# Kernel tuning notes

Measured on AMD Instinct MI355X. Metric: run time of the kernel, lower is better.

Reference implementation:

```python
import jax, jax.numpy as jnp
import numpy as np

N_WIRES = 24
DIM = 2
N_LAYERS = 4  # brickwork layers -> 12+11+12+11 = 46 two-qubit gates


def _brick_pairs():
    pairs = []
    for layer in range(N_LAYERS):
        start = layer % 2
        for w in range(start, N_WIRES - 1, 2):
            pairs.append((w, w + 1))
    return np.asarray(pairs, dtype=np.int64)  # (46, 2)


def setup_inputs() -> dict:
    key = jax.random.key(0)
    k1, k2 = jax.random.split(key)
    gate_wires = _brick_pairs()
    n_gates = gate_wires.shape[0]
    # per-wire initial state vectors (AbstractState -> one free index per wire)
    states = jax.random.normal(k1, (N_WIRES, DIM), dtype=jnp.float32)
    # two-qubit gates, axis order (in0, out0, in1, out1) per subscripts_unitary
    gates = jax.random.normal(k2, (n_gates, DIM, DIM, DIM, DIM), dtype=jnp.float32)
    return {"states": states, "gates": gates, "gate_wires": gate_wires}


def reference(states, gates, gate_wires):
    # Equivalent to jnp.einsum(subscripts_unitary(circuit), *tensors):
    # outer-product of initial per-wire states, then sequential contraction
    # of each gate's input axes (0, 2) with the state's wire axes.
    n_wires = states.shape[0]
    wires = np.asarray(gate_wires)
    psi = states[0]
    for w in range(1, n_wires):  # fixed structural loop over wires
        psi = jnp.tensordot(psi, states[w], axes=0)  # -> (d,)*n_wires
    for g in range(gates.shape[0]):  # fixed structural loop over gates
        w0, w1 = int(wires[g, 0]), int(wires[g, 1])
        # gate axes: 0=in0, 1=out0, 2=in1, 3=out1
        psi = jnp.tensordot(gates[g], psi, axes=[[0, 2], [w0, w1]])
        # result axes: (out0, out1, remaining wires); restore wire ordering
        psi = jnp.moveaxis(psi, (0, 1), (w0, w1))
    return psi  # final statevector, shape (d,)*n_wires
```

## Files before the change

### kernel.cpp

```cpp
#include <hip/hip_runtime.h>
#include <hip/hip_bf16.h>


#define SWZ(j) ((j) ^ (((j) >> 6) & 15) ^ ((((j) >> 10) & 1) << 4))

template<int A>
__device__ __forceinline__ void gate_regs(float v[64], const float* __restrict__ g) {
  float m[16];
#pragma unroll
  for (int vv = 0; vv < 4; ++vv)
#pragma unroll
    for (int uu = 0; uu < 4; ++uu)
      m[vv * 4 + uu] = g[(uu >> 1) * 8 + (vv >> 1) * 4 + (uu & 1) * 2 + (vv & 1)];
  constexpr int S = 1 << A;
#pragma unroll
  for (int hi = 0; hi < (1 << (4 - A)); ++hi)
#pragma unroll
    for (int lo = 0; lo < S; ++lo) {
      const int base = (hi << (A + 2)) | lo;
      const float a0 = v[base], a1 = v[base + S], a2 = v[base + 2 * S], a3 = v[base + 3 * S];
      v[base]         = m[0]  * a0 + m[1]  * a1 + m[2]  * a2 + m[3]  * a3;
      v[base + S]     = m[4]  * a0 + m[5]  * a1 + m[6]  * a2 + m[7]  * a3;
      v[base + 2 * S] = m[8]  * a0 + m[9]  * a1 + m[10] * a2 + m[11] * a3;
      v[base + 3 * S] = m[12] * a0 + m[13] * a1 + m[14] * a2 + m[15] * a3;
    }
}

#define J_B(t, r)  (((r) << 8) | (t))
#define J_M(t, r)  ((((t) >> 4) << 10) | ((r) << 4) | ((t) & 15))
#define J_A(t, r)  (((t) << 6) | (r))
#define J_W(t, r)  ((((t) >> 5) << 11) | ((r) << 5) | ((t) & 31))

#define TRANSITION(JW, JR)                                   \
  do {                                                       \
    _Pragma("unroll")                                        \
    for (int r = 0; r < 64; ++r) tile[SWZ(JW(t, r))] = v[r]; \
    __syncthreads();                                         \
    _Pragma("unroll")                                        \
    for (int r = 0; r < 64; ++r) v[r] = tile[SWZ(JR(t, r))]; \
    __syncthreads();                                         \
  } while (0)

__global__ __launch_bounds__(256) void k_pass1(
    const float* __restrict__ states, const float* __restrict__ gates,
    float* __restrict__ out) {
  __shared__ float tile[16384];
  __shared__ float sLo[256];
  __shared__ float sHi[64];
  const int t = threadIdx.x;
  const int b = blockIdx.x;

  {
    float p = 1.f;
    for (int k = 0; k < 8; ++k) p *= states[(23 - k) * 2 + ((t >> k) & 1)];
    sLo[t] = p;
    if (t < 64) {
      float q = 1.f;
      for (int k = 0; k < 6; ++k) q *= states[(15 - k) * 2 + ((t >> k) & 1)];
      sHi[t] = q;
    }
  }
  float pref = 1.f;
  for (int k = 0; k < 10; ++k) pref *= states[(9 - k) * 2 + ((b >> k) & 1)];
  __syncthreads();

  float v[64];
  const float plT = pref * sLo[t];
#pragma unroll
  for (int r = 0; r < 64; ++r) v[r] = plT * sHi[r];

  gate_regs<4>(v, gates + 16 * 5);
  gate_regs<2>(v, gates + 16 * 6);
  gate_regs<0>(v, gates + 16 * 7);
  gate_regs<3>(v, gates + 16 * 17);
  gate_regs<1>(v, gates + 16 * 18);
  gate_regs<2>(v, gates + 16 * 29);

  TRANSITION(J_B, J_M);

  gate_regs<2>(v, gates + 16 * 8);
  gate_regs<0>(v, gates + 16 * 9);
  gate_regs<3>(v, gates + 16 * 19);
  gate_regs<1>(v, gates + 16 * 20);
  gate_regs<4>(v, gates + 16 * 30);
  gate_regs<2>(v, gates + 16 * 31);

  TRANSITION(J_M, J_A);

  gate_regs<2>(v, gates + 16 * 10);
  gate_regs<0>(v, gates + 16 * 11);
  gate_regs<3>(v, gates + 16 * 21);
  gate_regs<1>(v, gates + 16 * 22);
  gate_regs<4>(v, gates + 16 * 32);
  gate_regs<2>(v, gates + 16 * 33);
  gate_regs<0>(v, gates + 16 * 34);
  gate_regs<3>(v, gates + 16 * 44);
  gate_regs<1>(v, gates + 16 * 45);

  TRANSITION(J_A, J_W);

  gate_regs<4>(v, gates + 16 * 41);
  gate_regs<2>(v, gates + 16 * 42);
  gate_regs<0>(v, gates + 16 * 43);

  const long long ob = ((long long)b) << 14;
#pragma unroll
  for (int r = 0; r < 64; ++r) out[ob | J_W(t, r)] = v[r];
}

__global__ __launch_bounds__(256) void k_pass2a(
    const float* __restrict__ gates, float* __restrict__ out) {
  __shared__ float tile[16384];
  const int t = threadIdx.x;
  const int b = blockIdx.x;
  const long long base0 = (((long long)(b >> 4)) << 18) | ((long long)(b & 15) << 6);

  float v[64];
#pragma unroll
  for (int r = 0; r < 64; ++r) {
    const int j = J_B(t, r);
    v[r] = out[base0 | (((long long)(j >> 6)) << 10) | (j & 63)];
  }
  gate_regs<4>(v, gates + 16 * 3);
  gate_regs<2>(v, gates + 16 * 4);
  gate_regs<3>(v, gates + 16 * 15);
  gate_regs<1>(v, gates + 16 * 16);
  gate_regs<2>(v, gates + 16 * 27);
  gate_regs<0>(v, gates + 16 * 28);
  gate_regs<1>(v, gates + 16 * 39);

  TRANSITION(J_B, J_W);

  gate_regs<2>(v, gates + 16 * 40);

#pragma unroll
  for (int r = 0; r < 64; ++r) {
    const int j = J_W(t, r);
    out[base0 | (((long long)(j >> 6)) << 10) | (j & 63)] = v[r];
  }
}

__global__ __launch_bounds__(256) void k_pass2b(
    const float* __restrict__ gates, float* __restrict__ out) {
  __shared__ float tile[16384];
  const int t = threadIdx.x;
  const int b = blockIdx.x;

  float v[64];
#pragma unroll
  for (int r = 0; r < 64; ++r) {
    const int j = J_B(t, r);
    v[r] = out[(((long long)(j >> 5)) << 15) | ((long long)b << 5) | (j & 31)];
  }
  gate_regs<4>(v, gates + 16 * 0);
  gate_regs<2>(v, gates + 16 * 1);
  gate_regs<0>(v, gates + 16 * 2);
  gate_regs<3>(v, gates + 16 * 12);
  gate_regs<1>(v, gates + 16 * 13);
  gate_regs<4>(v, gates + 16 * 23);
  gate_regs<2>(v, gates + 16 * 24);
  gate_regs<3>(v, gates + 16 * 35);

  TRANSITION(J_B, J_W);

  gate_regs<2>(v, gates + 16 * 14);
  gate_regs<3>(v, gates + 16 * 25);
  gate_regs<1>(v, gates + 16 * 26);
  gate_regs<4>(v, gates + 16 * 36);
  gate_regs<2>(v, gates + 16 * 37);
  gate_regs<0>(v, gates + 16 * 38);

#pragma unroll
  for (int r = 0; r < 64; ++r) {
    const int j = J_W(t, r);
    out[(((long long)(j >> 5)) << 15) | ((long long)b << 5) | (j & 31)] = v[r];
  }
}

extern "C" void kernel_launch(void* const* d_in, const int* in_sizes, int n_in,
                              void* d_out, int out_size, void* d_ws, size_t ws_size,
                              hipStream_t stream) {
  const float* states = (const float*)d_in[0];
  const float* gates = (const float*)d_in[1];
  float* out = (float*)d_out;

  k_pass1<<<1024, 256, 0, stream>>>(states, gates, out);
  k_pass2a<<<1024, 256, 0, stream>>>(gates, out);
  k_pass2b<<<1024, 256, 0, stream>>>(gates, out);
}
```

Baseline: 201.2 us.

## Vectorize global loads/stores as float4 and use packed float2 gate math

Global reads and writes in all three passes now move 16 float4 values per thread instead of 64 scalar accesses. Extra shared-memory transitions (J_F, J_V layouts) are added so that each thread holds four contiguous low-index amplitudes, and gate applications are reordered across the transitions to match the new register layouts. The gate kernel is also rewritten to use two-wide float vectors, aiming at packed FMA instructions. This trades more LDS shuffles and barriers for wider, better-coalesced global traffic.

Measured after the change: 202.3 us. No clear change (+0.6%).

```diff
diff --git a/kernel.cpp b/kernel.cpp
--- a/kernel.cpp
+++ b/kernel.cpp
@@ -1,6 +1,8 @@
 #include <hip/hip_runtime.h>
 #include <hip/hip_bf16.h>
 
+
+typedef float v2f __attribute__((ext_vector_type(2)));
 
 #define SWZ(j) ((j) ^ (((j) >> 6) & 15) ^ ((((j) >> 10) & 1) << 4))
 
@@ -12,24 +14,45 @@
 #pragma unroll
     for (int uu = 0; uu < 4; ++uu)
       m[vv * 4 + uu] = g[(uu >> 1) * 8 + (vv >> 1) * 4 + (uu & 1) * 2 + (vv & 1)];
-  constexpr int S = 1 << A;
-#pragma unroll
-  for (int hi = 0; hi < (1 << (4 - A)); ++hi)
-#pragma unroll
-    for (int lo = 0; lo < S; ++lo) {
-      const int base = (hi << (A + 2)) | lo;
-      const float a0 = v[base], a1 = v[base + S], a2 = v[base + 2 * S], a3 = v[base + 3 * S];
-      v[base]         = m[0]  * a0 + m[1]  * a1 + m[2]  * a2 + m[3]  * a3;
-      v[base + S]     = m[4]  * a0 + m[5]  * a1 + m[6]  * a2 + m[7]  * a3;
-      v[base + 2 * S] = m[8]  * a0 + m[9]  * a1 + m[10] * a2 + m[11] * a3;
-      v[base + 3 * S] = m[12] * a0 + m[13] * a1 + m[14] * a2 + m[15] * a3;
+  if constexpr (A == 0) {
+    v2f m04 = {m[0], m[4]}, m15 = {m[1], m[5]}, m26 = {m[2], m[6]}, m37 = {m[3], m[7]};
+    v2f m8c = {m[8], m[12]}, m9d = {m[9], m[13]}, mae = {m[10], m[14]}, mbf = {m[11], m[15]};
+#pragma unroll
+    for (int q = 0; q < 16; ++q) {
+      const float a0 = v[4 * q], a1 = v[4 * q + 1], a2 = v[4 * q + 2], a3 = v[4 * q + 3];
+      v2f r01 = m04 * a0 + m15 * a1 + m26 * a2 + m37 * a3;
+      v2f r23 = m8c * a0 + m9d * a1 + mae * a2 + mbf * a3;
+      v[4 * q] = r01.x; v[4 * q + 1] = r01.y; v[4 * q + 2] = r23.x; v[4 * q + 3] = r23.y;
     }
+  } else {
+    constexpr int S = 1 << A;
+#pragma unroll
+    for (int hi = 0; hi < (1 << (4 - A)); ++hi)
+#pragma unroll
+      for (int lo2 = 0; lo2 < S / 2; ++lo2) {
+        const int base = (hi << (A + 2)) | (lo2 << 1);
+        v2f a0 = {v[base], v[base + 1]};
+        v2f a1 = {v[base + S], v[base + S + 1]};
+        v2f a2 = {v[base + 2 * S], v[base + 2 * S + 1]};
+        v2f a3 = {v[base + 3 * S], v[base + 3 * S + 1]};
+        v2f r0 = m[0] * a0 + m[1] * a1 + m[2] * a2 + m[3] * a3;
+        v2f r1 = m[4] * a0 + m[5] * a1 + m[6] * a2 + m[7] * a3;
+        v2f r2 = m[8] * a0 + m[9] * a1 + m[10] * a2 + m[11] * a3;
+        v2f r3 = m[12] * a0 + m[13] * a1 + m[14] * a2 + m[15] * a3;
+        v[base] = r0.x; v[base + 1] = r0.y;
+        v[base + S] = r1.x; v[base + S + 1] = r1.y;
+        v[base + 2 * S] = r2.x; v[base + 2 * S + 1] = r2.y;
+        v[base + 3 * S] = r3.x; v[base + 3 * S + 1] = r3.y;
+      }
+  }
 }
 
 #define J_B(t, r)  (((r) << 8) | (t))
 #define J_M(t, r)  ((((t) >> 4) << 10) | ((r) << 4) | ((t) & 15))
 #define J_A(t, r)  (((t) << 6) | (r))
 #define J_W(t, r)  ((((t) >> 5) << 11) | ((r) << 5) | ((t) & 31))
+#define J_F(t, r)  (((r) & 3) | ((t) << 2) | (((r) >> 2) << 10))
+#define J_V(t, r)  (((t) & 127) | ((r) << 7) | (((t) >> 7) << 13))
 
 #define TRANSITION(JW, JR)                                   \
   do {                                                       \
@@ -75,18 +98,14 @@
   gate_regs<3>(v, gates + 16 * 17);
   gate_regs<1>(v, gates + 16 * 18);
   gate_regs<2>(v, gates + 16 * 29);
-
   TRANSITION(J_B, J_M);
-
   gate_regs<2>(v, gates + 16 * 8);
   gate_regs<0>(v, gates + 16 * 9);
   gate_regs<3>(v, gates + 16 * 19);
   gate_regs<1>(v, gates + 16 * 20);
   gate_regs<4>(v, gates + 16 * 30);
   gate_regs<2>(v, gates + 16 * 31);
-
   TRANSITION(J_M, J_A);
-
   gate_regs<2>(v, gates + 16 * 10);
   gate_regs<0>(v, gates + 16 * 11);
   gate_regs<3>(v, gates + 16 * 21);
@@ -96,16 +115,18 @@
   gate_regs<0>(v, gates + 16 * 34);
   gate_regs<3>(v, gates + 16 * 44);
   gate_regs<1>(v, gates + 16 * 45);
-
   TRANSITION(J_A, J_W);
-
   gate_regs<4>(v, gates + 16 * 41);
   gate_regs<2>(v, gates + 16 * 42);
   gate_regs<0>(v, gates + 16 * 43);
+  TRANSITION(J_W, J_F);
 
   const long long ob = ((long long)b) << 14;
 #pragma unroll
-  for (int r = 0; r < 64; ++r) out[ob | J_W(t, r)] = v[r];
+  for (int c = 0; c < 16; ++c) {
+    float4 w = make_float4(v[4 * c], v[4 * c + 1], v[4 * c + 2], v[4 * c + 3]);
+    *(float4*)(&out[ob + (t << 2) + ((long long)c << 10)]) = w;
+  }
 }
 
 __global__ __launch_bounds__(256) void k_pass2a(
@@ -117,26 +138,25 @@
 
   float v[64];
 #pragma unroll
-  for (int r = 0; r < 64; ++r) {
-    const int j = J_B(t, r);
-    v[r] = out[base0 | (((long long)(j >> 6)) << 10) | (j & 63)];
+  for (int c = 0; c < 16; ++c) {
+    float4 x = *(const float4*)(&out[base0 + ((t & 15) << 2) + ((t >> 4) << 10) + ((long long)c << 14)]);
+    v[4 * c] = x.x; v[4 * c + 1] = x.y; v[4 * c + 2] = x.z; v[4 * c + 3] = x.w;
   }
   gate_regs<4>(v, gates + 16 * 3);
-  gate_regs<2>(v, gates + 16 * 4);
-  gate_regs<3>(v, gates + 16 * 15);
-  gate_regs<1>(v, gates + 16 * 16);
-  gate_regs<2>(v, gates + 16 * 27);
-  gate_regs<0>(v, gates + 16 * 28);
-  gate_regs<1>(v, gates + 16 * 39);
-
-  TRANSITION(J_B, J_W);
-
-  gate_regs<2>(v, gates + 16 * 40);
-
-#pragma unroll
-  for (int r = 0; r < 64; ++r) {
-    const int j = J_W(t, r);
-    out[base0 | (((long long)(j >> 6)) << 10) | (j & 63)] = v[r];
+  TRANSITION(J_F, J_V);
+  gate_regs<3>(v, gates + 16 * 4);
+  gate_regs<4>(v, gates + 16 * 15);
+  gate_regs<2>(v, gates + 16 * 16);
+  gate_regs<3>(v, gates + 16 * 27);
+  gate_regs<1>(v, gates + 16 * 28);
+  gate_regs<2>(v, gates + 16 * 39);
+  gate_regs<0>(v, gates + 16 * 40);
+  TRANSITION(J_V, J_F);
+
+#pragma unroll
+  for (int c = 0; c < 16; ++c) {
+    float4 w = make_float4(v[4 * c], v[4 * c + 1], v[4 * c + 2], v[4 * c + 3]);
+    *(float4*)(&out[base0 + ((t & 15) << 2) + ((t >> 4) << 10) + ((long long)c << 14)]) = w;
   }
 }
 
@@ -148,32 +168,32 @@
 
   float v[64];
 #pragma unroll
-  for (int r = 0; r < 64; ++r) {
-    const int j = J_B(t, r);
-    v[r] = out[(((long long)(j >> 5)) << 15) | ((long long)b << 5) | (j & 31)];
+  for (int c = 0; c < 16; ++c) {
+    float4 x = *(const float4*)(&out[((t & 7) << 2) + ((long long)b << 5) + ((t >> 3) << 15) + ((long long)c << 20)]);
+    v[4 * c] = x.x; v[4 * c + 1] = x.y; v[4 * c + 2] = x.z; v[4 * c + 3] = x.w;
   }
   gate_regs<4>(v, gates + 16 * 0);
   gate_regs<2>(v, gates + 16 * 1);
+  gate_regs<3>(v, gates + 16 * 12);
+  gate_regs<4>(v, gates + 16 * 23);
+  TRANSITION(J_F, J_B);
   gate_regs<0>(v, gates + 16 * 2);
-  gate_regs<3>(v, gates + 16 * 12);
   gate_regs<1>(v, gates + 16 * 13);
-  gate_regs<4>(v, gates + 16 * 23);
   gate_regs<2>(v, gates + 16 * 24);
   gate_regs<3>(v, gates + 16 * 35);
-
   TRANSITION(J_B, J_W);
-
   gate_regs<2>(v, gates + 16 * 14);
   gate_regs<3>(v, gates + 16 * 25);
   gate_regs<1>(v, gates + 16 * 26);
   gate_regs<4>(v, gates + 16 * 36);
   gate_regs<2>(v, gates + 16 * 37);
   gate_regs<0>(v, gates + 16 * 38);
-
-#pragma unroll
-  for (int r = 0; r < 64; ++r) {
-    const int j = J_W(t, r);
-    out[(((long long)(j >> 5)) << 15) | ((long long)b << 5) | (j & 31)] = v[r];
+  TRANSITION(J_W, J_F);
+
+#pragma unroll
+  for (int c = 0; c < 16; ++c) {
+    float4 w = make_float4(v[4 * c], v[4 * c + 1], v[4 * c + 2], v[4 * c + 3]);
+    *(float4*)(&out[((t & 7) << 2) + ((long long)b << 5) + ((t >> 3) << 15) + ((long long)c << 20)]) = w;
   }
 }
 
```

## Pack amplitudes into float2 vectors, halve LDS tile and vectorize global loads

Applied to the files above, without the earlier changes.

Stores each thread's 64 amplitudes as 32 float2 vectors so gate updates can use packed FMA instructions, with the qubit-to-register mappings remapped per stage. The LDS transpose is split into two half-sized rounds, which halves shared memory per block so that launch_bounds(256,4) can target four blocks per CU. The pass-2 kernels now load with float4 global reads and reorder gates across the transposes. The added barriers and extra LDS rounds add synchronisation cost, and the complex index remapping risks correctness errors.

New measurement: 261.7 us. 30.1% more time.

```diff
diff --git a/kernel.cpp b/kernel.cpp
--- a/kernel.cpp
+++ b/kernel.cpp
@@ -1,179 +1,213 @@
 #include <hip/hip_runtime.h>
-#include <hip/hip_bf16.h>
-
+
+
+typedef float v2f __attribute__((ext_vector_type(2)));
 
 #define SWZ(j) ((j) ^ (((j) >> 6) & 15) ^ ((((j) >> 10) & 1) << 4))
-
-template<int A>
-__device__ __forceinline__ void gate_regs(float v[64], const float* __restrict__ g) {
+#define DEL(x, S) (((x) & ((1 << (S)) - 1)) | (((x) >> ((S) + 1)) << (S)))
+#define AMP_LD(r) (((r) & 1) ? w[(r) >> 1].y : w[(r) >> 1].x)
+#define AMP_ST(r, val) do { if ((r) & 1) w[(r) >> 1].y = (val); else w[(r) >> 1].x = (val); } while (0)
+
+template<int B0, int B1>
+__device__ __forceinline__ void gate_v2(v2f w[32], const float* __restrict__ g) {
   float m[16];
 #pragma unroll
   for (int vv = 0; vv < 4; ++vv)
 #pragma unroll
     for (int uu = 0; uu < 4; ++uu)
       m[vv * 4 + uu] = g[(uu >> 1) * 8 + (vv >> 1) * 4 + (uu & 1) * 2 + (vv & 1)];
-  constexpr int S = 1 << A;
-#pragma unroll
-  for (int hi = 0; hi < (1 << (4 - A)); ++hi)
-#pragma unroll
-    for (int lo = 0; lo < S; ++lo) {
-      const int base = (hi << (A + 2)) | lo;
-      const float a0 = v[base], a1 = v[base + S], a2 = v[base + 2 * S], a3 = v[base + 3 * S];
-      v[base]         = m[0]  * a0 + m[1]  * a1 + m[2]  * a2 + m[3]  * a3;
-      v[base + S]     = m[4]  * a0 + m[5]  * a1 + m[6]  * a2 + m[7]  * a3;
-      v[base + 2 * S] = m[8]  * a0 + m[9]  * a1 + m[10] * a2 + m[11] * a3;
-      v[base + 3 * S] = m[12] * a0 + m[13] * a1 + m[14] * a2 + m[15] * a3;
-    }
-}
-
-#define J_B(t, r)  (((r) << 8) | (t))
-#define J_M(t, r)  ((((t) >> 4) << 10) | ((r) << 4) | ((t) & 15))
-#define J_A(t, r)  (((t) << 6) | (r))
-#define J_W(t, r)  ((((t) >> 5) << 11) | ((r) << 5) | ((t) & 31))
-
-#define TRANSITION(JW, JR)                                   \
-  do {                                                       \
-    _Pragma("unroll")                                        \
-    for (int r = 0; r < 64; ++r) tile[SWZ(JW(t, r))] = v[r]; \
-    __syncthreads();                                         \
-    _Pragma("unroll")                                        \
-    for (int r = 0; r < 64; ++r) v[r] = tile[SWZ(JR(t, r))]; \
-    __syncthreads();                                         \
+  if constexpr (B0 != 0 && B1 != 0) {
+    constexpr int S1 = 1 << B0, S0 = 1 << B1;
+#pragma unroll
+    for (int b = 0; b < 64; ++b) {
+      if (b & (S0 | S1 | 1)) continue;
+      v2f A0 = w[b >> 1], A1 = w[(b + S1) >> 1], A2 = w[(b + S0) >> 1], A3 = w[(b + S0 + S1) >> 1];
+      w[b >> 1]             = m[0] * A0 + m[1] * A1 + m[2] * A2 + m[3] * A3;
+      w[(b + S1) >> 1]      = m[4] * A0 + m[5] * A1 + m[6] * A2 + m[7] * A3;
+      w[(b + S0) >> 1]      = m[8] * A0 + m[9] * A1 + m[10] * A2 + m[11] * A3;
+      w[(b + S0 + S1) >> 1] = m[12] * A0 + m[13] * A1 + m[14] * A2 + m[15] * A3;
+    }
+  } else if constexpr (B0 == 0) {
+    constexpr int S0 = 1 << B1;
+    v2f m04 = {m[0], m[4]}, m15 = {m[1], m[5]}, m26 = {m[2], m[6]}, m37 = {m[3], m[7]};
+    v2f m8c = {m[8], m[12]}, m9d = {m[9], m[13]}, mae = {m[10], m[14]}, mbf = {m[11], m[15]};
+#pragma unroll
+    for (int b = 0; b < 64; ++b) {
+      if (b & (S0 | 1)) continue;
+      v2f p = w[b >> 1], q = w[(b + S0) >> 1];
+      w[b >> 1]        = m04 * p.x + m15 * p.y + m26 * q.x + m37 * q.y;
+      w[(b + S0) >> 1] = m8c * p.x + m9d * p.y + mae * q.x + mbf * q.y;
+    }
+  } else {
+    constexpr int S1 = 1 << B0;
+    v2f m08 = {m[0], m[8]}, m19 = {m[1], m[9]}, m2a = {m[2], m[10]}, m3b = {m[3], m[11]};
+    v2f m4c = {m[4], m[12]}, m5d = {m[5], m[13]}, m6e = {m[6], m[14]}, m7f = {m[7], m[15]};
+#pragma unroll
+    for (int b = 0; b < 64; ++b) {
+      if (b & (S1 | 1)) continue;
+      v2f p = w[b >> 1], q = w[(b + S1) >> 1];
+      w[b >> 1]        = m08 * p.x + m19 * q.x + m2a * p.y + m3b * q.y;
+      w[(b + S1) >> 1] = m4c * p.x + m5d * q.x + m6e * p.y + m7f * q.y;
+    }
+  }
+}
+
+#define JB1(t, r) ((t) | ((r) << 8))
+#define JM1(t, r) (((t) & 15) | ((((r) >> 1) & 15) << 4) | (((r) & 1) << 8) | (((r) >> 5) << 9) | (((t) >> 4) << 10))
+#define JA1(t, r) (((r) & 3) | ((((r) >> 3) & 7) << 2) | ((((r) >> 2) & 1) << 5) | ((t) << 6))
+#define JW1(t, r) (((t) & 31) | ((((r) >> 2) & 1) << 5) | (((r) & 1) << 6) | ((((r) >> 1) & 1) << 7) | ((((r) >> 3) & 7) << 8) | (((t) >> 5) << 11))
+#define JF(t, r)  (((r) & 3) | ((t) << 2) | (((r) >> 2) << 10))
+#define JV(t, r)  (((t) & 127) | (((r) & 1) << 7) | ((((r) >> 1) & 1) << 8) | ((((r) >> 3) & 1) << 9) | ((((r) >> 2) & 1) << 10) | ((((r) >> 4) & 3) << 11) | (((t) >> 7) << 13))
+#define JW2(t, r) (((t) & 31) | ((((r) >> 1) & 7) << 5) | (((r) & 1) << 8) | ((((r) >> 4) & 3) << 9) | (((t) >> 5) << 11))
+
+#define TRANS(JW, JR, S, RBIT)                                        \
+  do {                                                                \
+    _Pragma("unroll")                                                 \
+    for (int r = 0; r < 64; ++r) if ((((r) >> (RBIT)) & 1) == 0)      \
+      buf[DEL(SWZ(JW(t, r)), S)] = AMP_LD(r);                         \
+    __syncthreads();                                                  \
+    _Pragma("unroll")                                                 \
+    for (int r = 0; r < 64; ++r) if ((((r) >> (RBIT)) & 1) == 0)      \
+      AMP_ST(r, buf[DEL(SWZ(JR(t, r)), S)]);                          \
+    __syncthreads();                                                  \
+    _Pragma("unroll")                                                 \
+    for (int r = 0; r < 64; ++r) if ((((r) >> (RBIT)) & 1) == 1)      \
+      buf[DEL(SWZ(JW(t, r)), S)] = AMP_LD(r);                         \
+    __syncthreads();                                                  \
+    _Pragma("unroll")                                                 \
+    for (int r = 0; r < 64; ++r) if ((((r) >> (RBIT)) & 1) == 1)      \
+      AMP_ST(r, buf[DEL(SWZ(JR(t, r)), S)]);                          \
+    __syncthreads();                                                  \
   } while (0)
 
-__global__ __launch_bounds__(256) void k_pass1(
+__global__ __launch_bounds__(256, 4) void k_pass1(
     const float* __restrict__ states, const float* __restrict__ gates,
     float* __restrict__ out) {
-  __shared__ float tile[16384];
-  __shared__ float sLo[256];
-  __shared__ float sHi[64];
+  __shared__ float buf[8192];
   const int t = threadIdx.x;
   const int b = blockIdx.x;
 
   {
     float p = 1.f;
     for (int k = 0; k < 8; ++k) p *= states[(23 - k) * 2 + ((t >> k) & 1)];
-    sLo[t] = p;
+    buf[t] = p;
     if (t < 64) {
       float q = 1.f;
       for (int k = 0; k < 6; ++k) q *= states[(15 - k) * 2 + ((t >> k) & 1)];
-      sHi[t] = q;
+      buf[256 + t] = q;
     }
   }
   float pref = 1.f;
   for (int k = 0; k < 10; ++k) pref *= states[(9 - k) * 2 + ((b >> k) & 1)];
   __syncthreads();
 
-  float v[64];
-  const float plT = pref * sLo[t];
-#pragma unroll
-  for (int r = 0; r < 64; ++r) v[r] = plT * sHi[r];
-
-  gate_regs<4>(v, gates + 16 * 5);
-  gate_regs<2>(v, gates + 16 * 6);
-  gate_regs<0>(v, gates + 16 * 7);
-  gate_regs<3>(v, gates + 16 * 17);
-  gate_regs<1>(v, gates + 16 * 18);
-  gate_regs<2>(v, gates + 16 * 29);
-
-  TRANSITION(J_B, J_M);
-
-  gate_regs<2>(v, gates + 16 * 8);
-  gate_regs<0>(v, gates + 16 * 9);
-  gate_regs<3>(v, gates + 16 * 19);
-  gate_regs<1>(v, gates + 16 * 20);
-  gate_regs<4>(v, gates + 16 * 30);
-  gate_regs<2>(v, gates + 16 * 31);
-
-  TRANSITION(J_M, J_A);
-
-  gate_regs<2>(v, gates + 16 * 10);
-  gate_regs<0>(v, gates + 16 * 11);
-  gate_regs<3>(v, gates + 16 * 21);
-  gate_regs<1>(v, gates + 16 * 22);
-  gate_regs<4>(v, gates + 16 * 32);
-  gate_regs<2>(v, gates + 16 * 33);
-  gate_regs<0>(v, gates + 16 * 34);
-  gate_regs<3>(v, gates + 16 * 44);
-  gate_regs<1>(v, gates + 16 * 45);
-
-  TRANSITION(J_A, J_W);
-
-  gate_regs<4>(v, gates + 16 * 41);
-  gate_regs<2>(v, gates + 16 * 42);
-  gate_regs<0>(v, gates + 16 * 43);
+  v2f w[32];
+  const float plT = pref * buf[t];
+#pragma unroll
+  for (int i = 0; i < 32; ++i) {
+    w[i].x = plT * buf[256 + 2 * i];
+    w[i].y = plT * buf[256 + 2 * i + 1];
+  }
+  __syncthreads();
+
+  gate_v2<4, 5>(w, gates + 16 * 5);
+  gate_v2<2, 3>(w, gates + 16 * 6);
+  gate_v2<0, 1>(w, gates + 16 * 7);
+  gate_v2<3, 4>(w, gates + 16 * 17);
+  gate_v2<1, 2>(w, gates + 16 * 18);
+  gate_v2<2, 3>(w, gates + 16 * 29);
+  TRANS(JB1, JM1, 8, 0);
+  gate_v2<3, 4>(w, gates + 16 * 8);
+  gate_v2<1, 2>(w, gates + 16 * 9);
+  gate_v2<4, 0>(w, gates + 16 * 19);
+  gate_v2<2, 3>(w, gates + 16 * 20);
+  gate_v2<0, 5>(w, gates + 16 * 30);
+  gate_v2<3, 4>(w, gates + 16 * 31);
+  TRANS(JM1, JA1, 5, 2);
+  gate_v2<3, 4>(w, gates + 16 * 10);
+  gate_v2<0, 1>(w, gates + 16 * 11);
+  gate_v2<4, 5>(w, gates + 16 * 21);
+  gate_v2<1, 3>(w, gates + 16 * 22);
+  gate_v2<5, 2>(w, gates + 16 * 32);
+  gate_v2<3, 4>(w, gates + 16 * 33);
+  gate_v2<0, 1>(w, gates + 16 * 34);
+  gate_v2<4, 5>(w, gates + 16 * 44);
+  gate_v2<1, 3>(w, gates + 16 * 45);
+  TRANS(JA1, JW1, 5, 2);
+  gate_v2<4, 5>(w, gates + 16 * 41);
+  gate_v2<1, 3>(w, gates + 16 * 42);
+  gate_v2<2, 0>(w, gates + 16 * 43);
 
   const long long ob = ((long long)b) << 14;
 #pragma unroll
-  for (int r = 0; r < 64; ++r) out[ob | J_W(t, r)] = v[r];
-}
-
-__global__ __launch_bounds__(256) void k_pass2a(
+  for (int r = 0; r < 64; ++r) out[ob | JW1(t, r)] = AMP_LD(r);
+}
+
+__global__ __launch_bounds__(256, 4) void k_pass2a(
     const float* __restrict__ gates, float* __restrict__ out) {
-  __shared__ float tile[16384];
+  __shared__ float buf[8192];
   const int t = threadIdx.x;
   const int b = blockIdx.x;
   const long long base0 = (((long long)(b >> 4)) << 18) | ((long long)(b & 15) << 6);
 
-  float v[64];
+  v2f w[32];
+#pragma unroll
+  for (int c = 0; c < 16; ++c) {
+    float4 x = *(const float4*)(&out[base0 + ((t & 15) << 2) + ((t >> 4) << 10) + ((long long)c << 14)]);
+    w[2 * c] = (v2f){x.x, x.y};
+    w[2 * c + 1] = (v2f){x.z, x.w};
+  }
+  gate_v2<4, 5>(w, gates + 16 * 3);
+  TRANS(JF, JV, 10, 2);
+  gate_v2<2, 4>(w, gates + 16 * 4);
+  gate_v2<4, 5>(w, gates + 16 * 15);
+  gate_v2<3, 2>(w, gates + 16 * 16);
+  gate_v2<2, 4>(w, gates + 16 * 27);
+  gate_v2<1, 3>(w, gates + 16 * 28);
+  gate_v2<3, 2>(w, gates + 16 * 39);
+  gate_v2<0, 1>(w, gates + 16 * 40);
+
 #pragma unroll
   for (int r = 0; r < 64; ++r) {
-    const int j = J_B(t, r);
-    v[r] = out[base0 | (((long long)(j >> 6)) << 10) | (j & 63)];
-  }
-  gate_regs<4>(v, gates + 16 * 3);
-  gate_regs<2>(v, gates + 16 * 4);
-  gate_regs<3>(v, gates + 16 * 15);
-  gate_regs<1>(v, gates + 16 * 16);
-  gate_regs<2>(v, gates + 16 * 27);
-  gate_regs<0>(v, gates + 16 * 28);
-  gate_regs<1>(v, gates + 16 * 39);
-
-  TRANSITION(J_B, J_W);
-
-  gate_regs<2>(v, gates + 16 * 40);
-
-#pragma unroll
-  for (int r = 0; r < 64; ++r) {
-    const int j = J_W(t, r);
-    out[base0 | (((long long)(j >> 6)) << 10) | (j & 63)] = v[r];
-  }
-}
-
-__global__ __launch_bounds__(256) void k_pass2b(
+    const int j = JV(t, r);
+    out[base0 | (((long long)(j >> 6)) << 10) | (j & 63)] = AMP_LD(r);
+  }
+}
+
+__global__ __launch_bounds__(256, 4) void k_pass2b(
     const float* __restrict__ gates, float* __restrict__ out) {
-  __shared__ float tile[16384];
+  __shared__ float buf[8192];
   const int t = threadIdx.x;
   const int b = blockIdx.x;
 
-  float v[64];
+  v2f w[32];
+#pragma unroll
+  for (int c = 0; c < 16; ++c) {
+    float4 x = *(const float4*)(&out[((t & 7) << 2) + ((long long)b << 5) + ((t >> 3) << 15) + ((long long)c << 20)]);
+    w[2 * c] = (v2f){x.x, x.y};
+    w[2 * c + 1] = (v2f){x.z, x.w};
+  }
+  gate_v2<4, 5>(w, gates + 16 * 0);
+  gate_v2<2, 3>(w, gates + 16 * 1);
+  gate_v2<3, 4>(w, gates + 16 * 12);
+  gate_v2<4, 5>(w, gates + 16 * 23);
+  TRANS(JF, JB1, 10, 2);
+  gate_v2<0, 1>(w, gates + 16 * 2);
+  gate_v2<1, 2>(w, gates + 16 * 13);
+  gate_v2<2, 3>(w, gates + 16 * 24);
+  gate_v2<3, 4>(w, gates + 16 * 35);
+  TRANS(JB1, JW2, 8, 0);
+  gate_v2<3, 0>(w, gates + 16 * 14);
+  gate_v2<0, 4>(w, gates + 16 * 25);
+  gate_v2<2, 3>(w, gates + 16 * 26);
+  gate_v2<4, 5>(w, gates + 16 * 36);
+  gate_v2<3, 0>(w, gates + 16 * 37);
+  gate_v2<1, 2>(w, gates + 16 * 38);
+
 #pragma unroll
   for (int r = 0; r < 64; ++r) {
-    const int j = J_B(t, r);
-    v[r] = out[(((long long)(j >> 5)) << 15) | ((long long)b << 5) | (j & 31)];
-  }
-  gate_regs<4>(v, gates + 16 * 0);
-  gate_regs<2>(v, gates + 16 * 1);
-  gate_regs<0>(v, gates + 16 * 2);
-  gate_regs<3>(v, gates + 16 * 12);
-  gate_regs<1>(v, gates + 16 * 13);
-  gate_regs<4>(v, gates + 16 * 23);
-  gate_regs<2>(v, gates + 16 * 24);
-  gate_regs<3>(v, gates + 16 * 35);
-
-  TRANSITION(J_B, J_W);
-
-  gate_regs<2>(v, gates + 16 * 14);
-  gate_regs<3>(v, gates + 16 * 25);
-  gate_regs<1>(v, gates + 16 * 26);
-  gate_regs<4>(v, gates + 16 * 36);
-  gate_regs<2>(v, gates + 16 * 37);
-  gate_regs<0>(v, gates + 16 * 38);
-
-#pragma unroll
-  for (int r = 0; r < 64; ++r) {
-    const int j = J_W(t, r);
-    out[(((long long)(j >> 5)) << 15) | ((long long)b << 5) | (j & 31)] = v[r];
+    const int j = JW2(t, r);
+    out[(((long long)(j >> 5)) << 15) | ((long long)b << 5) | (j & 31)] = AMP_LD(r);
   }
 }
 
```
